# Kernel optimization log

Measured on AMD Instinct MI355X. Metric: run time of the kernel, lower is better.

The kernel has to match this reference:

```python
import jax, jax.numpy as jnp
import numpy as np

B, P, D, V = 8192, 32, 128, 100000  # batch, max path len, embed dim, label_num


def setup_inputs() -> dict:
    key = jax.random.key(0)
    k1, k2, k3, k4, k5, k6 = jax.random.split(key, 6)
    return {
        "hidden_": jax.random.normal(k1, (B, D), dtype=jnp.float32),
        "target": jax.random.randint(k2, (B,), 0, V, dtype=jnp.int64),
        "target_path": jax.random.randint(k3, (B, P), 0, V, dtype=jnp.int64),
        "target_path_len": jax.random.randint(k4, (B,), 1, P, dtype=jnp.int64),
        "target_code": jax.random.randint(k5, (B, P), 0, 2, dtype=jnp.int64),
        "embed_table": jax.random.normal(k6, (V, D), dtype=jnp.float32) * 0.02,
    }


def reference(hidden_, target, target_path, target_path_len, target_code, embed_table):
    # embeds: [B, P, D] gather of tree-node vectors along each label's path
    embeds = embed_table[target_path]
    # per-node score: sigmoid(<node_vec, hidden>) -> [B, P]
    score = jax.nn.sigmoid(jnp.einsum("bpd,bd->bp", embeds, hidden_))
    flag = target_code.astype(jnp.float32)
    # BCE-style per-node loss, exactly as the TF code writes it
    loss = -jnp.log(flag * score + (1.0 - flag) * (1.0 - score))
    # ragged path mask: positions < target_path_len are valid (tf.ragged.range + batch_gather)
    mask = (jnp.arange(P)[None, :] < target_path_len[:, None]).astype(jnp.float32)
    # reduce_mean over the ragged tensor = sum of valid losses / total valid count
    return jnp.sum(loss * mask) / jnp.sum(mask)
```

## Files before the change

kernel.cpp:

```cpp
#include <hip/hip_runtime.h>

#define BB 8192
#define PP 32
#define DD 128
#define RPB 8

__global__ __launch_bounds__(256) void hs_loss_kernel(
    const float* __restrict__ hidden,
    const int*   __restrict__ path,
    const int*   __restrict__ path_len,
    const int*   __restrict__ code,
    const float* __restrict__ embed,
    float2* __restrict__ partials)
{
    const int tid = threadIdx.x;
    const int p   = tid & 31;
    const int bl  = tid >> 5;
    const int b   = blockIdx.x * RPB + bl;

    __shared__ float hlds[RPB * DD];
    ((float4*)hlds)[tid] = ((const float4*)hidden)[b * (DD / 4) + p];

    const int  len   = path_len[b];
    const bool valid = (p < len);

    __syncthreads();

    float loss = 0.0f;
    if (valid) {
        const int idx = path[b * PP + p];
        const int cd  = code[b * PP + p];
        const float4* __restrict__ erow = (const float4*)(embed + (size_t)idx * DD);
        const float4* __restrict__ hrow = (const float4*)(hlds + bl * DD);

        float acc = 0.0f;
        #pragma unroll
        for (int c0 = 0; c0 < DD / 4; c0 += 8) {
            float4 e[8];
            #pragma unroll
            for (int j = 0; j < 8; ++j) e[j] = erow[c0 + j];
            #pragma unroll
            for (int j = 0; j < 8; ++j) {
                const float4 h = hrow[c0 + j];
                acc += e[j].x * h.x + e[j].y * h.y
                     + e[j].z * h.z + e[j].w * h.w;
            }
        }
        const float z = cd ? -acc : acc;
        loss = fmaxf(z, 0.0f) + __logf(1.0f + __expf(-fabsf(z)));
    }

    const unsigned long long bal = __ballot(valid);

    #pragma unroll
    for (int m = 1; m <= 32; m <<= 1) loss += __shfl_xor(loss, m);

    __shared__ float s_l[4], s_c[4];
    const int wv = tid >> 6;
    if ((tid & 63) == 0) {
        s_l[wv] = loss;
        s_c[wv] = (float)__popcll(bal);
    }
    __syncthreads();
    if (tid == 0) {
        partials[blockIdx.x] = make_float2(s_l[0] + s_l[1] + s_l[2] + s_l[3],
                                           s_c[0] + s_c[1] + s_c[2] + s_c[3]);
    }
}

__global__ __launch_bounds__(1024) void hs_finalize_kernel(
    const float2* __restrict__ partials, float* __restrict__ out)
{
    const int tid = threadIdx.x;
    const float2 v = partials[tid];
    float ls = v.x, cs = v.y;
    #pragma unroll
    for (int m = 1; m <= 32; m <<= 1) {
        ls += __shfl_xor(ls, m);
        cs += __shfl_xor(cs, m);
    }
    __shared__ float s_l[16], s_c[16];
    const int wave = tid >> 6;
    if ((tid & 63) == 0) { s_l[wave] = ls; s_c[wave] = cs; }
    __syncthreads();
    if (tid == 0) {
        float L = 0.0f, C = 0.0f;
        #pragma unroll
        for (int w = 0; w < 16; ++w) { L += s_l[w]; C += s_c[w]; }
        out[0] = L / C;
    }
}

extern "C" void kernel_launch(void* const* d_in, const int* in_sizes, int n_in,
                              void* d_out, int out_size, void* d_ws, size_t ws_size,
                              hipStream_t stream) {
    const float* hidden   = (const float*)d_in[0];
    const int*   path     = (const int*)d_in[2];
    const int*   path_len = (const int*)d_in[3];
    const int*   code     = (const int*)d_in[4];
    const float* embed    = (const float*)d_in[5];
    float*  out      = (float*)d_out;
    float2* partials = (float2*)d_ws;

    hs_loss_kernel<<<BB / RPB, 256, 0, stream>>>(hidden, path, path_len, code,
                                                 embed, partials);
    hs_finalize_kernel<<<1, 1024, 0, stream>>>(partials, out);
}
```

Measured before the change: 108.4 us.

## Stage gathered embedding rows cooperatively in LDS with coalesced half-wave loads

Each block now handles two batch rows. A half-wave loads each 512-byte embedding row, so loads are coalesced instead of one thread streaming a whole row. Rows are staged in 32KB of LDS, then four waves split the dot product across D with a rotated index to avoid bank conflicts and combine the results through shared memory. The cost is more LDS per block (lower occupancy), an extra barrier, and twice as many partials for the finalize kernel to reduce.

```diff
diff --git a/kernel.cpp b/kernel.cpp
--- a/kernel.cpp
+++ b/kernel.cpp
@@ -3,7 +3,6 @@
 #define BB 8192
 #define PP 32
 #define DD 128
-#define RPB 8
 
 __global__ __launch_bounds__(256) void hs_loss_kernel(
     const float* __restrict__ hidden,
@@ -13,58 +12,70 @@
     const float* __restrict__ embed,
     float2* __restrict__ partials)
 {
-    const int tid = threadIdx.x;
-    const int p   = tid & 31;
-    const int bl  = tid >> 5;
-    const int b   = blockIdx.x * RPB + bl;
+    const int tid  = threadIdx.x;
+    const int lane = tid & 63;
+    const int w    = tid >> 6;
+    const int b0   = blockIdx.x * 2;
 
-    __shared__ float hlds[RPB * DD];
-    ((float4*)hlds)[tid] = ((const float4*)hidden)[b * (DD / 4) + p];
+    __shared__ float elds[64 * DD];
+    __shared__ float hlds[2 * DD];
+    __shared__ float part[4][64];
 
-    const int  len   = path_len[b];
-    const bool valid = (p < len);
+    hlds[tid] = hidden[(size_t)b0 * DD + tid];
 
+    const int lenA = path_len[b0];
+    const int lenB = path_len[b0 + 1];
+
+    {
+        const int brow  = w >> 1;
+        const int pbase = (w & 1) * 16;
+        const int lenw  = brow ? lenB : lenA;
+        const int half  = lane >> 5;
+        const int hl    = lane & 31;
+        #pragma unroll
+        for (int j = 0; j < 8; ++j) {
+            const int pj = pbase + 2 * j;
+            if (pj < lenw) {
+                const int p   = min(pj + half, lenw - 1);
+                const int idx = path[(b0 + brow) * PP + p];
+                const float4 e = ((const float4*)(embed + (size_t)idx * DD))[hl];
+                const int slot = brow * 32 + pj + half;
+                ((float4*)elds)[slot * 32 + hl] = e;
+            }
+        }
+    }
     __syncthreads();
 
-    float loss = 0.0f;
-    if (valid) {
-        const int idx = path[b * PP + p];
-        const int cd  = code[b * PP + p];
-        const float4* __restrict__ erow = (const float4*)(embed + (size_t)idx * DD);
-        const float4* __restrict__ hrow = (const float4*)(hlds + bl * DD);
+    float acc = 0.0f;
+    {
+        const float4* hrow = (const float4*)(hlds + (lane >> 5) * DD);
+        #pragma unroll
+        for (int j = 0; j < 8; ++j) {
+            const int c = 8 * w + ((j + lane) & 7);
+            const float4 e = ((const float4*)elds)[lane * 32 + c];
+            const float4 h = hrow[c];
+            acc += e.x * h.x + e.y * h.y + e.z * h.z + e.w * h.w;
+        }
+    }
+    part[w][lane] = acc;
+    __syncthreads();
 
-        float acc = 0.0f;
+    if (tid < 64) {
+        const float dot = part[0][tid] + part[1][tid]
+                        + part[2][tid] + part[3][tid];
+        const int p   = tid & 31;
+        const int bl  = tid >> 5;
+        const int len = bl ? lenB : lenA;
+        float loss = 0.0f;
+        if (p < len) {
+            const int cd = code[(b0 + bl) * PP + p];
+            const float z = cd ? -dot : dot;
+            loss = fmaxf(z, 0.0f) + __logf(1.0f + __expf(-fabsf(z)));
+        }
         #pragma unroll
-        for (int c0 = 0; c0 < DD / 4; c0 += 8) {
-            float4 e[8];
-            #pragma unroll
-            for (int j = 0; j < 8; ++j) e[j] = erow[c0 + j];
-            #pragma unroll
-            for (int j = 0; j < 8; ++j) {
-                const float4 h = hrow[c0 + j];
-                acc += e[j].x * h.x + e[j].y * h.y
-                     + e[j].z * h.z + e[j].w * h.w;
-            }
-        }
-        const float z = cd ? -acc : acc;
-        loss = fmaxf(z, 0.0f) + __logf(1.0f + __expf(-fabsf(z)));
-    }
-
-    const unsigned long long bal = __ballot(valid);
-
-    #pragma unroll
-    for (int m = 1; m <= 32; m <<= 1) loss += __shfl_xor(loss, m);
-
-    __shared__ float s_l[4], s_c[4];
-    const int wv = tid >> 6;
-    if ((tid & 63) == 0) {
-        s_l[wv] = loss;
-        s_c[wv] = (float)__popcll(bal);
-    }
-    __syncthreads();
-    if (tid == 0) {
-        partials[blockIdx.x] = make_float2(s_l[0] + s_l[1] + s_l[2] + s_l[3],
-                                           s_c[0] + s_c[1] + s_c[2] + s_c[3]);
+        for (int m = 1; m <= 32; m <<= 1) loss += __shfl_xor(loss, m);
+        if (tid == 0)
+            partials[blockIdx.x] = make_float2(loss, (float)(lenA + lenB));
     }
 }
 
@@ -72,8 +83,13 @@
     const float2* __restrict__ partials, float* __restrict__ out)
 {
     const int tid = threadIdx.x;
-    const float2 v = partials[tid];
-    float ls = v.x, cs = v.y;
+    float ls = 0.0f, cs = 0.0f;
+    #pragma unroll
+    for (int k = 0; k < (BB / 2) / 1024; ++k) {
+        const float2 v = partials[tid + k * 1024];
+        ls += v.x;
+        cs += v.y;
+    }
     #pragma unroll
     for (int m = 1; m <= 32; m <<= 1) {
         ls += __shfl_xor(ls, m);
@@ -86,7 +102,7 @@
     if (tid == 0) {
         float L = 0.0f, C = 0.0f;
         #pragma unroll
-        for (int w = 0; w < 16; ++w) { L += s_l[w]; C += s_c[w]; }
+        for (int wv = 0; wv < 16; ++wv) { L += s_l[wv]; C += s_c[wv]; }
         out[0] = L / C;
     }
 }
@@ -102,7 +118,7 @@
     float*  out      = (float*)d_out;
     float2* partials = (float2*)d_ws;
 
-    hs_loss_kernel<<<BB / RPB, 256, 0, stream>>>(hidden, path, path_len, code,
-                                                 embed, partials);
+    hs_loss_kernel<<<BB / 2, 256, 0, stream>>>(hidden, path, path_len, code,
+                                               embed, partials);
     hs_finalize_kernel<<<1, 1024, 0, stream>>>(partials, out);
 }
```

Result: slower. 119.6 us (+10.3%).

## Cooperatively gather embedding rows with 16 lanes per row for coalesced loads

Applied to the files above, without the earlier changes.

Before, each thread read a whole 512-byte embedding row by itself, so a wavefront's loads were scattered. Now 16 lanes share each row: every lane loads two float4 chunks, and the partial dot products are reduced through a padded LDS transpose. This gives coalesced 256-byte segments per row and removes the block-wide syncthreads, since each wave writes its own partial to a finalize step that now sums four times as many partials. The LDS transpose has no explicit wave barrier, so it relies on wave-synchronous execution, and the path-length mask becomes a per-row branch inside the unrolled loop.

```diff
diff --git a/kernel.cpp b/kernel.cpp
--- a/kernel.cpp
+++ b/kernel.cpp
@@ -3,7 +3,6 @@
 #define BB 8192
 #define PP 32
 #define DD 128
-#define RPB 8
 
 __global__ __launch_bounds__(256) void hs_loss_kernel(
     const float* __restrict__ hidden,
@@ -14,66 +13,68 @@
     float2* __restrict__ partials)
 {
     const int tid = threadIdx.x;
-    const int p   = tid & 31;
-    const int bl  = tid >> 5;
-    const int b   = blockIdx.x * RPB + bl;
+    const int w   = tid >> 6;
+    const int l   = tid & 63;
+    const int ql  = l & 15;
+    const int b0  = blockIdx.x * 8 + w * 2;
+    const int b   = b0 + (l >> 5);
 
-    __shared__ float hlds[RPB * DD];
-    ((float4*)hlds)[tid] = ((const float4*)hidden)[b * (DD / 4) + p];
+    __shared__ float plds[4][64 * 17];
+    float* const myp = plds[w];
 
-    const int  len   = path_len[b];
-    const bool valid = (p < len);
+    const int   idx_all = path[b0 * PP + l];
+    const int   cd_all  = code[b0 * PP + l];
+    const int   len     = path_len[b];
+    const float4 h0 = ((const float4*)hidden)[b * (DD / 4) + ql];
+    const float4 h1 = ((const float4*)hidden)[b * (DD / 4) + 16 + ql];
 
-    __syncthreads();
+    const int pbase = (l & 16);
 
+    #pragma unroll
+    for (int j = 0; j < 16; ++j) {
+        const int p   = pbase + j;
+        const int pid = (l & 48) + j;
+        const int idx = __shfl(idx_all, pid);
+        float partial = 0.0f;
+        if (p < len) {
+            const float4* erow = (const float4*)(embed + (size_t)idx * DD);
+            const float4 e0 = erow[ql];
+            const float4 e1 = erow[16 + ql];
+            partial = e0.x * h0.x + e0.y * h0.y + e0.z * h0.z + e0.w * h0.w
+                    + e1.x * h1.x + e1.y * h1.y + e1.z * h1.z + e1.w * h1.w;
+        }
+        myp[pid * 17 + ql] = partial;
+    }
+
+    float dot = 0.0f;
+    #pragma unroll
+    for (int k = 0; k < 16; ++k) dot += myp[l * 17 + k];
+
+    const bool valid = (l & 31) < len;
     float loss = 0.0f;
     if (valid) {
-        const int idx = path[b * PP + p];
-        const int cd  = code[b * PP + p];
-        const float4* __restrict__ erow = (const float4*)(embed + (size_t)idx * DD);
-        const float4* __restrict__ hrow = (const float4*)(hlds + bl * DD);
-
-        float acc = 0.0f;
-        #pragma unroll
-        for (int c0 = 0; c0 < DD / 4; c0 += 8) {
-            float4 e[8];
-            #pragma unroll
-            for (int j = 0; j < 8; ++j) e[j] = erow[c0 + j];
-            #pragma unroll
-            for (int j = 0; j < 8; ++j) {
-                const float4 h = hrow[c0 + j];
-                acc += e[j].x * h.x + e[j].y * h.y
-                     + e[j].z * h.z + e[j].w * h.w;
-            }
-        }
-        const float z = cd ? -acc : acc;
+        const float z = cd_all ? -dot : dot;
         loss = fmaxf(z, 0.0f) + __logf(1.0f + __expf(-fabsf(z)));
     }
-
     const unsigned long long bal = __ballot(valid);
-
     #pragma unroll
     for (int m = 1; m <= 32; m <<= 1) loss += __shfl_xor(loss, m);
-
-    __shared__ float s_l[4], s_c[4];
-    const int wv = tid >> 6;
-    if ((tid & 63) == 0) {
-        s_l[wv] = loss;
-        s_c[wv] = (float)__popcll(bal);
-    }
-    __syncthreads();
-    if (tid == 0) {
-        partials[blockIdx.x] = make_float2(s_l[0] + s_l[1] + s_l[2] + s_l[3],
-                                           s_c[0] + s_c[1] + s_c[2] + s_c[3]);
-    }
+    if (l == 0)
+        partials[blockIdx.x * 4 + w] =
+            make_float2(loss, (float)__popcll(bal));
 }
 
 __global__ __launch_bounds__(1024) void hs_finalize_kernel(
     const float2* __restrict__ partials, float* __restrict__ out)
 {
     const int tid = threadIdx.x;
-    const float2 v = partials[tid];
-    float ls = v.x, cs = v.y;
+    float ls = 0.0f, cs = 0.0f;
+    #pragma unroll
+    for (int k = 0; k < 4; ++k) {
+        const float2 v = partials[tid + k * 1024];
+        ls += v.x;
+        cs += v.y;
+    }
     #pragma unroll
     for (int m = 1; m <= 32; m <<= 1) {
         ls += __shfl_xor(ls, m);
@@ -86,7 +87,7 @@
     if (tid == 0) {
         float L = 0.0f, C = 0.0f;
         #pragma unroll
-        for (int w = 0; w < 16; ++w) { L += s_l[w]; C += s_c[w]; }
+        for (int wv = 0; wv < 16; ++wv) { L += s_l[wv]; C += s_c[wv]; }
         out[0] = L / C;
     }
 }
@@ -102,7 +103,7 @@
     float*  out      = (float*)d_out;
     float2* partials = (float2*)d_ws;
 
-    hs_loss_kernel<<<BB / RPB, 256, 0, stream>>>(hidden, path, path_len, code,
-                                                 embed, partials);
+    hs_loss_kernel<<<BB / 8, 256, 0, stream>>>(hidden, path, path_len, code,
+                                               embed, partials);
     hs_finalize_kernel<<<1, 1024, 0, stream>>>(partials, out);
 }
```

New measurement: 101.5 us. 6.4% less time.
